# Optimization experiments

Measured on AMD Instinct MI355X. Metric: run time of the kernel, lower is better.

The kernel has to match this reference:

```python
import jax, jax.numpy as jnp
import numpy as np


def setup_inputs() -> dict:
    key = jax.random.key(0)
    x = jax.random.normal(key, (1024, 65536), dtype=jnp.float32)
    return {"x": x, "k": 64}


def reference(x, k):
    # BatchTopK: ReLU, then keep the k*batch largest activations across the
    # ENTIRE flattened batch, zeroing everything else.
    acts = jax.nn.relu(x)
    flat = acts.reshape(-1)                      # [batch * d_sae]
    k_total = k * x.shape[0]
    vals, idx = jax.lax.top_k(flat, k_total)     # global selection
    out = jnp.zeros_like(flat).at[idx].set(vals) # scatter back
    return out.reshape(acts.shape)
```

## Files before the change

### kernel.cpp

```cpp
#include <hip/hip_runtime.h>
#include <stdint.h>


#define HDR_CURSOR 0
#define HDR_FLAG   1
#define HDR_THR    2
#define HDR_ICUT   3
#define CAND_OFF   4096
#define LDS_STAGE  2048
#define ROWS       1024u
#define SPEC       3.0f

__global__ void k_init(uint32_t* hdr, uint32_t force_flag) {
  if (threadIdx.x < 64u) hdr[threadIdx.x] = 0u;
  if (threadIdx.x == 0u) hdr[HDR_FLAG] = force_flag;
}

__global__ __launch_bounds__(256) void k_zero_scan(
    float4* __restrict__ out4, float* __restrict__ out,
    const float4* __restrict__ x4, const float* __restrict__ x,
    uint2* __restrict__ cand, uint32_t* __restrict__ hdr,
    uint32_t cap, uint32_t n4, uint32_t n, uint32_t half) {
  uint32_t role = blockIdx.x & 1u;
  uint32_t bid  = blockIdx.x >> 1;
  uint32_t stride = half * 256u;
  uint32_t tail0 = n4 * 4u;

  if (role == 0u) {
    const float4 z = make_float4(0.f, 0.f, 0.f, 0.f);
    for (uint32_t i = bid * 256u + threadIdx.x; i < n4; i += stride)
      out4[i] = z;
    if (bid == 0u && threadIdx.x < (n - tail0))
      out[tail0 + threadIdx.x] = 0.f;
    return;
  }

  __shared__ uint32_t s_cnt;
  __shared__ uint32_t s_base;
  __shared__ uint2 s_buf[LDS_STAGE];
  if (threadIdx.x == 0u) s_cnt = 0u;
  __syncthreads();

  for (uint32_t i = bid * 256u + threadIdx.x; i < n4; i += stride) {
    float4 a = x4[i];
    bool has = (a.x >= SPEC) || (a.y >= SPEC) || (a.z >= SPEC) || (a.w >= SPEC);
    if (__ballot(has ? 1 : 0)) {
      uint32_t gi = i * 4u;
      if (a.x >= SPEC) { uint32_t p = atomicAdd(&s_cnt, 1u); if (p < LDS_STAGE) s_buf[p] = make_uint2(__float_as_uint(a.x), gi); }
      if (a.y >= SPEC) { uint32_t p = atomicAdd(&s_cnt, 1u); if (p < LDS_STAGE) s_buf[p] = make_uint2(__float_as_uint(a.y), gi + 1u); }
      if (a.z >= SPEC) { uint32_t p = atomicAdd(&s_cnt, 1u); if (p < LDS_STAGE) s_buf[p] = make_uint2(__float_as_uint(a.z), gi + 2u); }
      if (a.w >= SPEC) { uint32_t p = atomicAdd(&s_cnt, 1u); if (p < LDS_STAGE) s_buf[p] = make_uint2(__float_as_uint(a.w), gi + 3u); }
    }
  }
  if (bid == 0u && threadIdx.x < (n - tail0)) {
    uint32_t gi = tail0 + threadIdx.x;
    float v = x[gi];
    if (v >= SPEC) { uint32_t p = atomicAdd(&s_cnt, 1u); if (p < LDS_STAGE) s_buf[p] = make_uint2(__float_as_uint(v), gi); }
  }
  __syncthreads();
  uint32_t cnt = s_cnt;
  if (cnt == 0u) return;
  uint32_t wcnt = cnt < (uint32_t)LDS_STAGE ? cnt : (uint32_t)LDS_STAGE;
  if (threadIdx.x == 0u) {
    s_base = atomicAdd(&hdr[HDR_CURSOR], cnt);
    if (cnt > (uint32_t)LDS_STAGE) atomicOr(&hdr[HDR_FLAG], 1u);
  }
  __syncthreads();
  uint32_t base = s_base;
  for (uint32_t j = threadIdx.x; j < wcnt; j += blockDim.x) {
    uint32_t g = base + j;
    if (g < cap) cand[g] = s_buf[j];
  }
  if (threadIdx.x == 0u && base + wcnt > cap) atomicOr(&hdr[HDR_FLAG], 1u);
}

__global__ __launch_bounds__(1024) void k_select(
    const uint2* __restrict__ cand, uint32_t* __restrict__ hdr,
    const int* __restrict__ kptr, uint32_t cap) {
  __shared__ uint32_t hist[2048];
  __shared__ uint32_t s_sel, s_rank, s_eqcnt, s_icut;
  __shared__ uint32_t eq_idx[4096];
  uint32_t tid = threadIdx.x;
  uint32_t K = (uint32_t)kptr[0] * ROWS;
  uint32_t M = hdr[HDR_CURSOR];
  if (hdr[HDR_FLAG] != 0u || M > cap || M < K) {
    if (tid == 0u) hdr[HDR_FLAG] = 1u;
    return;
  }
  if (K == 0u) {
    if (tid == 0u) { hdr[HDR_THR] = 0xFFFFFFFFu; hdr[HDR_ICUT] = 0xFFFFFFFFu; }
    return;
  }
  const uint4* __restrict__ cand4 = (const uint4*)cand;
  uint32_t M2 = M >> 1;
  uint32_t R = K;
  uint32_t prefix = 0u;
  for (int lvl = 0; lvl < 3; ++lvl) {
    uint32_t shift = (lvl == 0) ? 21u : (lvl == 1 ? 10u : 0u);
    uint32_t nb = (lvl == 2) ? 1024u : 2048u;
    for (uint32_t b = tid; b < nb; b += 1024u) hist[b] = 0u;
    __syncthreads();
    for (uint32_t j = tid; j < M2; j += 1024u) {
      uint4 c = cand4[j];
      uint32_t k0 = c.x, k1 = c.z;
      bool v0 = true, v1 = true;
      if (lvl == 1) { v0 = ((k0 >> 21) == prefix); v1 = ((k1 >> 21) == prefix); }
      if (lvl == 2) { v0 = ((k0 >> 10) == prefix); v1 = ((k1 >> 10) == prefix); }
      if (v0) atomicAdd(&hist[(k0 >> shift) & (nb - 1u)], 1u);
      if (v1) atomicAdd(&hist[(k1 >> shift) & (nb - 1u)], 1u);
    }
    if (tid == 0u && (M & 1u)) {
      uint32_t key = cand[M - 1u].x;
      bool v = true;
      if (lvl == 1) v = ((key >> 21) == prefix);
      if (lvl == 2) v = ((key >> 10) == prefix);
      if (v) atomicAdd(&hist[(key >> shift) & (nb - 1u)], 1u);
    }
    __syncthreads();
    if (tid < 64u) {
      uint32_t seg = nb >> 6;
      uint32_t base = tid * seg;
      uint32_t lanesum = 0u;
      for (uint32_t j = 0; j < seg; ++j) lanesum += hist[base + j];
      uint32_t s = lanesum;
      for (int d = 1; d < 64; d <<= 1) {
        uint32_t v = (uint32_t)__shfl_down((int)s, d, 64);
        if ((int)tid + d < 64) s += v;
      }
      uint32_t above = s - lanesum;
      if (above < R && above + lanesum >= R) {
        uint32_t r = R - above;
        uint32_t cum = 0u;
        for (int j = (int)seg - 1; j >= 0; --j) {
          uint32_t c = hist[base + (uint32_t)j];
          if (cum + c >= r) { s_sel = base + (uint32_t)j; s_rank = r - cum; break; }
          cum += c;
        }
      }
    }
    __syncthreads();
    uint32_t sel = s_sel;
    R = s_rank;
    if (lvl == 0) prefix = sel;
    else if (lvl == 1) prefix = (prefix << 11) | sel;
    else prefix = (prefix << 10) | sel;
  }
  uint32_t thr_key = prefix;
  uint32_t E = hist[thr_key & 1023u];
  uint32_t T = R;
  uint32_t icut = 0xFFFFFFFFu;
  if (T < E) {
    if (tid == 0u) { s_eqcnt = 0u; s_icut = 0xFFFFFFFFu; }
    __syncthreads();
    for (uint32_t i = tid; i < M; i += 1024u) {
      uint2 c = cand[i];
      if (c.x == thr_key) { uint32_t p = atomicAdd(&s_eqcnt, 1u); if (p < 4096u) eq_idx[p] = c.y; }
    }
    __syncthreads();
    if (s_eqcnt > 4096u) {
      if (tid == 0u) hdr[HDR_FLAG] = 1u;
      return;
    }
    uint32_t ec = s_eqcnt;
    for (uint32_t e = tid; e < ec; e += 1024u) {
      uint32_t me = eq_idx[e];
      uint32_t rank = 0u;
      for (uint32_t j = 0; j < ec; ++j) rank += (eq_idx[j] < me) ? 1u : 0u;
      if (rank == T - 1u) s_icut = me;
    }
    __syncthreads();
    icut = s_icut;
  }
  if (tid == 0u) { hdr[HDR_THR] = thr_key; hdr[HDR_ICUT] = icut; }
}

__global__ __launch_bounds__(256) void k_scatter(
    const uint2* __restrict__ cand, const uint32_t* __restrict__ hdr,
    float* __restrict__ out, uint32_t cap) {
  if (hdr[HDR_FLAG] != 0u) return;
  uint32_t M = hdr[HDR_CURSOR]; if (M > cap) M = cap;
  uint32_t thr = hdr[HDR_THR], icut = hdr[HDR_ICUT];
  uint32_t stride = gridDim.x * blockDim.x;
  for (uint32_t i = blockIdx.x * blockDim.x + threadIdx.x; i < M; i += stride) {
    uint2 c = cand[i];
    if (c.x > thr || (c.x == thr && c.y <= icut)) out[c.y] = __uint_as_float(c.x);
  }
}

__global__ __launch_bounds__(1024) void k_fallback(
    const float* __restrict__ x, float* __restrict__ out,
    const int* __restrict__ kptr, const uint32_t* __restrict__ hdr, uint32_t n) {
  if (hdr[HDR_FLAG] == 0u) return;
  __shared__ uint32_t hist[2048];
  __shared__ uint32_t s_sel, s_rank, s_found, s_eqcnt, s_icut;
  __shared__ uint32_t eq_idx[4096];
  uint32_t tid = threadIdx.x;
  uint32_t K = (uint32_t)kptr[0] * ROWS;
  uint32_t prefix = 0u;
  uint32_t R = K;
  bool zero_thr = (K == 0u);
  for (int lvl = 0; lvl < 3 && !zero_thr; ++lvl) {
    uint32_t shift = (lvl == 0) ? 21u : (lvl == 1 ? 10u : 0u);
    uint32_t nb = (lvl == 2) ? 1024u : 2048u;
    for (uint32_t b = tid; b < nb; b += 1024u) hist[b] = 0u;
    __syncthreads();
    for (uint32_t i = tid; i < n; i += 1024u) {
      float v = x[i];
      uint32_t key = (v > 0.f) ? __float_as_uint(v) : 0u;
      bool valid = (key != 0u);
      if (lvl == 1) valid = valid && ((key >> 21) == prefix);
      if (lvl == 2) valid = valid && ((key >> 10) == prefix);
      if (valid) atomicAdd(&hist[(key >> shift) & (nb - 1u)], 1u);
    }
    __syncthreads();
    if (tid == 0u) {
      uint32_t cum = 0u, sel = 0u, rr = R, found = 0u;
      for (int b = (int)nb - 1; b >= 0; --b) {
        uint32_t c = hist[b];
        if (cum + c >= R) { sel = (uint32_t)b; rr = R - cum; found = 1u; break; }
        cum += c;
      }
      s_sel = sel; s_rank = rr; s_found = found;
    }
    __syncthreads();
    if (s_found == 0u) {
      zero_thr = true;
    } else {
      uint32_t sel = s_sel;
      R = s_rank;
      if (lvl == 0) prefix = sel;
      else if (lvl == 1) prefix = (prefix << 11) | sel;
      else prefix = (prefix << 10) | sel;
    }
    __syncthreads();
  }
  uint32_t thr_key = zero_thr ? 0u : prefix;
  uint32_t icut = 0xFFFFFFFFu;
  if (!zero_thr) {
    uint32_t E = hist[thr_key & 1023u];
    uint32_t T = R;
    if (T < E) {
      if (tid == 0u) { s_eqcnt = 0u; s_icut = 0xFFFFFFFFu; }
      __syncthreads();
      for (uint32_t i = tid; i < n; i += 1024u) {
        float v = x[i];
        if (v > 0.f && __float_as_uint(v) == thr_key) {
          uint32_t p = atomicAdd(&s_eqcnt, 1u);
          if (p < 4096u) eq_idx[p] = i;
        }
      }
      __syncthreads();
      uint32_t ec = s_eqcnt < 4096u ? s_eqcnt : 4096u;
      for (uint32_t e = tid; e < ec; e += 1024u) {
        uint32_t me = eq_idx[e];
        uint32_t rank = 0u;
        for (uint32_t j = 0; j < ec; ++j) rank += (eq_idx[j] < me) ? 1u : 0u;
        if (rank == T - 1u) s_icut = me;
      }
      __syncthreads();
      icut = s_icut;
    }
  }
  for (uint32_t i = tid; i < n; i += 1024u) {
    float v = x[i];
    uint32_t key = (v > 0.f) ? __float_as_uint(v) : 0u;
    bool keep = (key > thr_key) || (key != 0u && key == thr_key && i <= icut);
    out[i] = keep ? v : 0.f;
  }
}

extern "C" void kernel_launch(void* const* d_in, const int* in_sizes, int n_in,
                              void* d_out, int out_size, void* d_ws, size_t ws_size,
                              hipStream_t stream) {
  const float* x = (const float*)d_in[0];
  const int* kptr = (const int*)d_in[1];
  float* out = (float*)d_out;
  uint32_t n = (uint32_t)in_sizes[0];
  uint32_t n4 = n >> 2;

  uint32_t* hdr = (uint32_t*)d_ws;
  uint2* cand = (uint2*)((char*)d_ws + CAND_OFF);
  uint32_t cap = (ws_size > (size_t)CAND_OFF) ? (uint32_t)((ws_size - CAND_OFF) / 8) : 0u;
  uint32_t force = (cap < 131072u) ? 1u : 0u;

  const uint32_t HALF = 2048u;
  k_init<<<1, 64, 0, stream>>>(hdr, force);
  k_zero_scan<<<2u * HALF, 256, 0, stream>>>((float4*)out, out, (const float4*)x, x,
                                             cand, hdr, cap, n4, n, HALF);
  k_select<<<1, 1024, 0, stream>>>(cand, hdr, kptr, cap);
  k_fallback<<<1, 1024, 0, stream>>>(x, out, kptr, hdr, n);
  k_scatter<<<256, 256, 0, stream>>>(cand, hdr, out, cap);
}
```

Before: 563.1 us.

## Build global candidate histogram during scan and select threshold from one bucket

The scan kernel now adds each candidate to a global 2048-bin histogram keyed on float bits above 3.0. The single-block select kernel reads that histogram to find the threshold bin, collects only that bin's candidates into LDS, and ranks them exactly by value and index. This replaces three full histogram passes plus a tie pass over all candidates in one block. In exchange it adds global atomics in the scan, and it falls back to the slow path if the target bin is the overflow bin or holds more than 6144 entries.

```diff
diff --git a/kernel.cpp b/kernel.cpp
--- a/kernel.cpp
+++ b/kernel.cpp
@@ -6,13 +6,26 @@
 #define HDR_FLAG   1
 #define HDR_THR    2
 #define HDR_ICUT   3
-#define CAND_OFF   4096
+#define HIST_OFF   4096
+#define CAND_OFF   16384
+#define NBINS      2048u
+#define BUCKET_CAP 6144u
 #define LDS_STAGE  2048
 #define ROWS       1024u
 #define SPEC       3.0f
-
-__global__ void k_init(uint32_t* hdr, uint32_t force_flag) {
-  if (threadIdx.x < 64u) hdr[threadIdx.x] = 0u;
+#define BASE_BITS  0x40400000u
+
+__device__ __forceinline__ uint32_t bin_of(uint32_t key) {
+  uint32_t off = key - BASE_BITS;
+  uint32_t b = off >> 12;
+  return b < NBINS ? b : (NBINS - 1u);
+}
+
+__global__ void k_init(uint32_t* hdr, uint32_t* ghist, uint32_t force_flag) {
+  for (uint32_t i = threadIdx.x; i < 64u + NBINS; i += 256u) {
+    if (i < 64u) hdr[i] = 0u;
+    else ghist[i - 64u] = 0u;
+  }
   if (threadIdx.x == 0u) hdr[HDR_FLAG] = force_flag;
 }
 
@@ -20,6 +33,7 @@
     float4* __restrict__ out4, float* __restrict__ out,
     const float4* __restrict__ x4, const float* __restrict__ x,
     uint2* __restrict__ cand, uint32_t* __restrict__ hdr,
+    uint32_t* __restrict__ ghist,
     uint32_t cap, uint32_t n4, uint32_t n, uint32_t half) {
   uint32_t role = blockIdx.x & 1u;
   uint32_t bid  = blockIdx.x >> 1;
@@ -69,17 +83,22 @@
   uint32_t base = s_base;
   for (uint32_t j = threadIdx.x; j < wcnt; j += blockDim.x) {
     uint32_t g = base + j;
-    if (g < cap) cand[g] = s_buf[j];
+    if (g < cap) {
+      uint2 c = s_buf[j];
+      cand[g] = c;
+      atomicAdd(&ghist[bin_of(c.x)], 1u);
+    }
   }
   if (threadIdx.x == 0u && base + wcnt > cap) atomicOr(&hdr[HDR_FLAG], 1u);
 }
 
 __global__ __launch_bounds__(1024) void k_select(
     const uint2* __restrict__ cand, uint32_t* __restrict__ hdr,
+    const uint32_t* __restrict__ ghist,
     const int* __restrict__ kptr, uint32_t cap) {
-  __shared__ uint32_t hist[2048];
-  __shared__ uint32_t s_sel, s_rank, s_eqcnt, s_icut;
-  __shared__ uint32_t eq_idx[4096];
+  __shared__ uint32_t h[NBINS];
+  __shared__ uint32_t s_sel, s_rank, s_bcnt;
+  __shared__ uint2 bkt[BUCKET_CAP];
   uint32_t tid = threadIdx.x;
   uint32_t K = (uint32_t)kptr[0] * ROWS;
   uint32_t M = hdr[HDR_CURSOR];
@@ -91,87 +110,60 @@
     if (tid == 0u) { hdr[HDR_THR] = 0xFFFFFFFFu; hdr[HDR_ICUT] = 0xFFFFFFFFu; }
     return;
   }
+  h[tid] = ghist[tid];
+  h[tid + 1024u] = ghist[tid + 1024u];
+  if (tid == 0u) s_bcnt = 0u;
+  __syncthreads();
+  if (tid < 64u) {
+    uint32_t seg = NBINS >> 6;
+    uint32_t base = tid * seg;
+    uint32_t lanesum = 0u;
+    for (uint32_t j = 0; j < seg; ++j) lanesum += h[base + j];
+    uint32_t s = lanesum;
+    for (int d = 1; d < 64; d <<= 1) {
+      uint32_t v = (uint32_t)__shfl_down((int)s, d, 64);
+      if ((int)tid + d < 64) s += v;
+    }
+    uint32_t above = s - lanesum;
+    if (above < K && above + lanesum >= K) {
+      uint32_t r = K - above;
+      uint32_t cum = 0u;
+      for (int j = (int)seg - 1; j >= 0; --j) {
+        uint32_t c = h[base + (uint32_t)j];
+        if (cum + c >= r) { s_sel = base + (uint32_t)j; s_rank = r - cum; break; }
+        cum += c;
+      }
+    }
+  }
+  __syncthreads();
+  uint32_t bsel = s_sel;
+  uint32_t r = s_rank;
+  uint32_t E = h[bsel];
+  if (bsel == NBINS - 1u || E > BUCKET_CAP) {
+    if (tid == 0u) hdr[HDR_FLAG] = 1u;
+    return;
+  }
   const uint4* __restrict__ cand4 = (const uint4*)cand;
   uint32_t M2 = M >> 1;
-  uint32_t R = K;
-  uint32_t prefix = 0u;
-  for (int lvl = 0; lvl < 3; ++lvl) {
-    uint32_t shift = (lvl == 0) ? 21u : (lvl == 1 ? 10u : 0u);
-    uint32_t nb = (lvl == 2) ? 1024u : 2048u;
-    for (uint32_t b = tid; b < nb; b += 1024u) hist[b] = 0u;
-    __syncthreads();
-    for (uint32_t j = tid; j < M2; j += 1024u) {
-      uint4 c = cand4[j];
-      uint32_t k0 = c.x, k1 = c.z;
-      bool v0 = true, v1 = true;
-      if (lvl == 1) { v0 = ((k0 >> 21) == prefix); v1 = ((k1 >> 21) == prefix); }
-      if (lvl == 2) { v0 = ((k0 >> 10) == prefix); v1 = ((k1 >> 10) == prefix); }
-      if (v0) atomicAdd(&hist[(k0 >> shift) & (nb - 1u)], 1u);
-      if (v1) atomicAdd(&hist[(k1 >> shift) & (nb - 1u)], 1u);
-    }
-    if (tid == 0u && (M & 1u)) {
-      uint32_t key = cand[M - 1u].x;
-      bool v = true;
-      if (lvl == 1) v = ((key >> 21) == prefix);
-      if (lvl == 2) v = ((key >> 10) == prefix);
-      if (v) atomicAdd(&hist[(key >> shift) & (nb - 1u)], 1u);
-    }
-    __syncthreads();
-    if (tid < 64u) {
-      uint32_t seg = nb >> 6;
-      uint32_t base = tid * seg;
-      uint32_t lanesum = 0u;
-      for (uint32_t j = 0; j < seg; ++j) lanesum += hist[base + j];
-      uint32_t s = lanesum;
-      for (int d = 1; d < 64; d <<= 1) {
-        uint32_t v = (uint32_t)__shfl_down((int)s, d, 64);
-        if ((int)tid + d < 64) s += v;
-      }
-      uint32_t above = s - lanesum;
-      if (above < R && above + lanesum >= R) {
-        uint32_t r = R - above;
-        uint32_t cum = 0u;
-        for (int j = (int)seg - 1; j >= 0; --j) {
-          uint32_t c = hist[base + (uint32_t)j];
-          if (cum + c >= r) { s_sel = base + (uint32_t)j; s_rank = r - cum; break; }
-          cum += c;
-        }
-      }
-    }
-    __syncthreads();
-    uint32_t sel = s_sel;
-    R = s_rank;
-    if (lvl == 0) prefix = sel;
-    else if (lvl == 1) prefix = (prefix << 11) | sel;
-    else prefix = (prefix << 10) | sel;
-  }
-  uint32_t thr_key = prefix;
-  uint32_t E = hist[thr_key & 1023u];
-  uint32_t T = R;
-  uint32_t icut = 0xFFFFFFFFu;
-  if (T < E) {
-    if (tid == 0u) { s_eqcnt = 0u; s_icut = 0xFFFFFFFFu; }
-    __syncthreads();
-    for (uint32_t i = tid; i < M; i += 1024u) {
-      uint2 c = cand[i];
-      if (c.x == thr_key) { uint32_t p = atomicAdd(&s_eqcnt, 1u); if (p < 4096u) eq_idx[p] = c.y; }
-    }
-    __syncthreads();
-    if (s_eqcnt > 4096u) {
-      if (tid == 0u) hdr[HDR_FLAG] = 1u;
-      return;
-    }
-    uint32_t ec = s_eqcnt;
-    for (uint32_t e = tid; e < ec; e += 1024u) {
-      uint32_t me = eq_idx[e];
-      uint32_t rank = 0u;
-      for (uint32_t j = 0; j < ec; ++j) rank += (eq_idx[j] < me) ? 1u : 0u;
-      if (rank == T - 1u) s_icut = me;
-    }
-    __syncthreads();
-    icut = s_icut;
-  }
-  if (tid == 0u) { hdr[HDR_THR] = thr_key; hdr[HDR_ICUT] = icut; }
+  for (uint32_t j = tid; j < M2; j += 1024u) {
+    uint4 c = cand4[j];
+    if (bin_of(c.x) == bsel) { uint32_t p = atomicAdd(&s_bcnt, 1u); if (p < BUCKET_CAP) bkt[p] = make_uint2(c.x, c.y); }
+    if (bin_of(c.z) == bsel) { uint32_t p = atomicAdd(&s_bcnt, 1u); if (p < BUCKET_CAP) bkt[p] = make_uint2(c.z, c.w); }
+  }
+  if (tid == 0u && (M & 1u)) {
+    uint2 c = cand[M - 1u];
+    if (bin_of(c.x) == bsel) { uint32_t p = atomicAdd(&s_bcnt, 1u); if (p < BUCKET_CAP) bkt[p] = c; }
+  }
+  __syncthreads();
+  for (uint32_t e = tid; e < E; e += 1024u) {
+    uint2 me = bkt[e];
+    uint32_t rank = 0u;
+    for (uint32_t j = 0; j < E; ++j) {
+      uint2 o = bkt[j];
+      rank += (o.x > me.x || (o.x == me.x && o.y < me.y)) ? 1u : 0u;
+    }
+    if (rank == r - 1u) { hdr[HDR_THR] = me.x; hdr[HDR_ICUT] = me.y; }
+  }
 }
 
 __global__ __launch_bounds__(256) void k_scatter(
@@ -279,15 +271,16 @@
   uint32_t n4 = n >> 2;
 
   uint32_t* hdr = (uint32_t*)d_ws;
+  uint32_t* ghist = (uint32_t*)((char*)d_ws + HIST_OFF);
   uint2* cand = (uint2*)((char*)d_ws + CAND_OFF);
   uint32_t cap = (ws_size > (size_t)CAND_OFF) ? (uint32_t)((ws_size - CAND_OFF) / 8) : 0u;
   uint32_t force = (cap < 131072u) ? 1u : 0u;
 
   const uint32_t HALF = 2048u;
-  k_init<<<1, 64, 0, stream>>>(hdr, force);
+  k_init<<<1, 256, 0, stream>>>(hdr, ghist, force);
   k_zero_scan<<<2u * HALF, 256, 0, stream>>>((float4*)out, out, (const float4*)x, x,
-                                             cand, hdr, cap, n4, n, HALF);
-  k_select<<<1, 1024, 0, stream>>>(cand, hdr, kptr, cap);
+                                             cand, hdr, ghist, cap, n4, n, HALF);
+  k_select<<<1, 1024, 0, stream>>>(cand, hdr, ghist, kptr, cap);
   k_fallback<<<1, 1024, 0, stream>>>(x, out, kptr, hdr, n);
   k_scatter<<<256, 256, 0, stream>>>(cand, hdr, out, cap);
 }
```

New measurement: 496.6 us. -11.8%, faster.
